# Performance work log

Measured on AMD Instinct MI355X. Metric: run time of the kernel, lower is better.

## Reference

```python
import jax, jax.numpy as jnp
import numpy as np
import math

# ---- static configuration (matches init_kwargs) ----
METADATA = [64, 48, 32]   # channels per l = 0,1,2
MAX_L = 3                 # order_out
N_BATCH = 32768
fact = math.factorial

def _cg_complex(l1, m1, l2, m2, l3, m3):
    # Clebsch-Gordan coefficient <l1 m1 l2 m2 | l3 m3> via Racah formula
    if m1 + m2 != m3 or l3 < abs(l1 - l2) or l3 > l1 + l2:
        return 0.0
    pre = math.sqrt((2*l3+1) * fact(l1+l2-l3) * fact(l1-l2+l3) * fact(-l1+l2+l3) / fact(l1+l2+l3+1))
    pre *= math.sqrt(fact(l1+m1)*fact(l1-m1)*fact(l2+m2)*fact(l2-m2)*fact(l3+m3)*fact(l3-m3))
    kmin = max(0, l2-l3-m1, l1-l3+m2)
    kmax = min(l1+l2-l3, l1-m1, l2+m2)
    s = 0.0
    for k in range(kmin, kmax+1):
        s += (-1)**k / (fact(k)*fact(l1+l2-l3-k)*fact(l1-m1-k)*fact(l2+m2-k)*fact(l3-l2+m1+k)*fact(l3-l1-m2+k))
    return pre * s

def _U(l):
    # complex->real spherical harmonic change of basis, rows = real m', cols = complex m
    U = np.zeros((2*l+1, 2*l+1), dtype=np.complex128)
    for m in range(-l, l+1):
        r = m + l
        if m > 0:
            U[r, m+l] = (-1)**m / math.sqrt(2.0); U[r, -m+l] = 1.0/math.sqrt(2.0)
        elif m == 0:
            U[r, l] = 1.0
        else:
            U[r, m+l] = 1j/math.sqrt(2.0); U[r, -m+l] = -1j*(-1)**m/math.sqrt(2.0)
    return U

def _real_cg(l1, l2, l3):
    Cc = np.zeros((2*l1+1, 2*l2+1, 2*l3+1))
    for m1 in range(-l1, l1+1):
        for m2 in range(-l2, l2+1):
            for m3 in range(-l3, l3+1):
                Cc[m1+l1, m2+l2, m3+l3] = _cg_complex(l1, m1, l2, m2, l3, m3)
    T = np.einsum('am,bn,co,mno->abc', _U(l1), _U(l2), _U(l3).conj(), Cc.astype(np.complex128))
    T = T.imag if np.abs(T.imag).max() > np.abs(T.real).max() else T.real
    return np.ascontiguousarray(T).astype(np.float32)

# ---- static index structures ----
L_IN = len(METADATA)
OFF_IN = np.concatenate([[0], np.cumsum([METADATA[l]*(2*l+1) for l in range(L_IN)])]).astype(np.int64)
DIM_IN = int(OFF_IN[-1])  # 368
PATHS = []
for l1 in range(L_IN):
    for l2 in range(L_IN):
        for l3 in range(abs(l1-l2), min(l1+l2, MAX_L)+1):
            PATHS.append((l1, l2, l3, min(METADATA[l1], METADATA[l2])))
MD_OV = [0]*(MAX_L+1)
for (_, _, l3, ch) in PATHS:
    MD_OV[l3] = max(MD_OV[l3], ch)
OFF_OUT = np.concatenate([[0], np.cumsum([MD_OV[l]*(2*l+1) for l in range(MAX_L+1)])]).astype(np.int64)
DIM_OUT = int(OFF_OUT[-1])  # 672
CG = {(l1, l2, l3): jnp.asarray(_real_cg(l1, l2, l3)) for (l1, l2, l3, _) in PATHS}

_mix_id, _scat = [], []
_base = 0
for (l1, l2, l3, ch) in PATHS:
    for i in range(ch):
        for m in range(2*l3+1):
            _mix_id.append(_base + i)
            _scat.append(int(OFF_OUT[l3]) + i*(2*l3+1) + m)
    _base += ch
MIX_ID = jnp.asarray(np.array(_mix_id, dtype=np.int64))
SCATTER = jnp.asarray(np.array(_scat, dtype=np.int64))
N_MIX = _base  # 688

_chan_in = []
_cb = 0
for l in range(L_IN):
    for i in range(METADATA[l]):
        _chan_in += [_cb + i]*(2*l+1)
    _cb += METADATA[l]
CHAN_IN = jnp.asarray(np.array(_chan_in, dtype=np.int64))
N_KEEP = _cb  # 144
_kin, _kout = [], []
for l in range(L_IN):
    cp = min(METADATA[l], MD_OV[l])
    for i in range(cp):
        for m in range(2*l+1):
            _kin.append(int(OFF_IN[l]) + i*(2*l+1) + m)
            _kout.append(int(OFF_OUT[l]) + i*(2*l+1) + m)
KEEP_IN = jnp.asarray(np.array(_kin, dtype=np.int64))
KEEP_OUT = jnp.asarray(np.array(_kout, dtype=np.int64))

SQ3 = math.sqrt(3.0)

def setup_inputs() -> dict:
    key = jax.random.key(0)
    k1, k2, k3 = jax.random.split(key, 3)
    x = jax.random.normal(k1, (N_BATCH, DIM_IN), dtype=jnp.float32)
    keep_coeff = jax.random.uniform(k2, (N_KEEP,), minval=-SQ3, maxval=SQ3, dtype=jnp.float32)
    mix_coeff = jax.random.uniform(k3, (N_MIX,), minval=-SQ3, maxval=SQ3, dtype=jnp.float32)
    return {"x": x, "keep_coeff": keep_coeff, "mix_coeff": mix_coeff}

def reference(x, keep_coeff, mix_coeff):
    n = x.shape[0]
    # keep path: per-channel coeff broadcast over m components
    x_keep = x * keep_coeff[CHAN_IN]  # [N, 368]
    # CG tensor-product self-coupling (diagonal channel pairing per path)
    tps = []
    for (l1, l2, l3, ch) in PATHS:
        x1 = x[:, OFF_IN[l1]:OFF_IN[l1]+ch*(2*l1+1)].reshape(n, ch, 2*l1+1)
        x2 = x[:, OFF_IN[l2]:OFF_IN[l2]+ch*(2*l2+1)].reshape(n, ch, 2*l2+1)
        tps.append(jnp.einsum('nia,nib,abm->nim', x1, x2, CG[(l1, l2, l3)]).reshape(n, -1))
    cat = jnp.concatenate(tps, axis=1)  # [N, 2576] non-overlapped TP output
    cat = cat * 0.5 * mix_coeff[MIX_ID]
    # scatter (index_add) into overlapped output layout
    out = jnp.zeros((n, DIM_OUT), dtype=x.dtype).at[:, SCATTER].add(cat)
    # gather + add of keep path (index_select + add_)
    out = out.at[:, KEEP_OUT].add(x_keep[:, KEEP_IN])
    return out
```

## Files before the change

kernel.cpp:

```cpp
#include <hip/hip_runtime.h>


namespace cgc {

struct cplx { double re, im; };
constexpr cplx cmul(cplx a, cplx b){ return {a.re*b.re - a.im*b.im, a.re*b.im + a.im*b.re}; }

constexpr double cfact(int n){ double r = 1.0; for (int i = 2; i <= n; ++i) r *= i; return r; }
constexpr double cabsd(double x){ return x < 0 ? -x : x; }

constexpr double csqrtd(double x){
  if (x <= 0.0) return 0.0;
  double g = x > 1.0 ? x : 1.0;
  for (int i = 0; i < 48; ++i) g = 0.5*(g + x/g);
  return g;
}

constexpr double SQRT2 = csqrtd(2.0);

constexpr double cg_complex(int l1,int m1,int l2,int m2,int l3,int m3){
  if (m1 + m2 != m3) return 0.0;
  int lo = l1 > l2 ? l1 - l2 : l2 - l1;
  if (l3 < lo || l3 > l1 + l2) return 0.0;
  double pre = csqrtd((2*l3+1) * cfact(l1+l2-l3)*cfact(l1-l2+l3)*cfact(-l1+l2+l3)/cfact(l1+l2+l3+1));
  pre *= csqrtd(cfact(l1+m1)*cfact(l1-m1)*cfact(l2+m2)*cfact(l2-m2)*cfact(l3+m3)*cfact(l3-m3));
  int kmin = 0;
  if (l2-l3-m1 > kmin) kmin = l2-l3-m1;
  if (l1-l3+m2 > kmin) kmin = l1-l3+m2;
  int kmax = l1+l2-l3;
  if (l1-m1 < kmax) kmax = l1-m1;
  if (l2+m2 < kmax) kmax = l2+m2;
  double s = 0.0;
  for (int k = kmin; k <= kmax; ++k){
    double d = cfact(k)*cfact(l1+l2-l3-k)*cfact(l1-m1-k)*cfact(l2+m2-k)
             * cfact(l3-l2+m1+k)*cfact(l3-l1-m2+k);
    s += ((k & 1) ? -1.0 : 1.0) / d;
  }
  return pre * s;
}

constexpr cplx Uent(int l, int r, int c){
  int m = r - l;
  if (m > 0){
    if (c ==  m + l) return { ((m & 1) ? -1.0 : 1.0)/SQRT2, 0.0 };
    if (c == -m + l) return { 1.0/SQRT2, 0.0 };
    return {0.0, 0.0};
  } else if (m == 0){
    if (c == l) return {1.0, 0.0};
    return {0.0, 0.0};
  } else {
    int ma = -m;
    if (c ==  m + l) return { 0.0, 1.0/SQRT2 };
    if (c == -m + l) return { 0.0, -(((ma & 1) ? -1.0 : 1.0))/SQRT2 };
    return {0.0, 0.0};
  }
}

template<int L1,int L2,int L3>
struct CGData { float w[(2*L1+1)*(2*L2+1)*(2*L3+1)]; };

template<int L1,int L2,int L3>
constexpr CGData<L1,L2,L3> make_cg(){
  constexpr int D1 = 2*L1+1, D2 = 2*L2+1, D3 = 2*L3+1;
  cplx U1[D1*D1] = {}; cplx U2[D2*D2] = {}; cplx U3c[D3*D3] = {};
  for (int r = 0; r < D1; ++r) for (int c = 0; c < D1; ++c) U1[r*D1+c] = Uent(L1, r, c);
  for (int r = 0; r < D2; ++r) for (int c = 0; c < D2; ++c) U2[r*D2+c] = Uent(L2, r, c);
  for (int r = 0; r < D3; ++r) for (int c = 0; c < D3; ++c){
    cplx u = Uent(L3, r, c); u.im = -u.im; U3c[r*D3+c] = u;
  }
  double Cc[D1*D2*D3] = {};
  for (int m1 = -L1; m1 <= L1; ++m1)
    for (int m2 = -L2; m2 <= L2; ++m2){
      int m3 = m1 + m2;
      if (m3 < -L3 || m3 > L3) continue;
      Cc[((m1+L1)*D2 + (m2+L2))*D3 + (m3+L3)] = cg_complex(L1,m1,L2,m2,L3,m3);
    }
  double re[D1*D2*D3] = {}; double im[D1*D2*D3] = {};
  for (int a = 0; a < D1; ++a)
    for (int b = 0; b < D2; ++b)
      for (int c = 0; c < D3; ++c){
        double sre = 0.0, sim = 0.0;
        for (int m = 0; m < D1; ++m)
          for (int n = 0; n < D2; ++n){
            int o = m + n - L1 - L2 + L3;
            if (o < 0 || o >= D3) continue;
            double cc = Cc[(m*D2+n)*D3 + o];
            if (cc == 0.0) continue;
            cplx p = cmul(cmul(U1[a*D1+m], U2[b*D2+n]), U3c[c*D3+o]);
            sre += p.re * cc; sim += p.im * cc;
          }
        re[(a*D2+b)*D3+c] = sre; im[(a*D2+b)*D3+c] = sim;
      }
  double mre = 0.0, mim = 0.0;
  for (int k = 0; k < D1*D2*D3; ++k){
    if (cabsd(re[k]) > mre) mre = cabsd(re[k]);
    if (cabsd(im[k]) > mim) mim = cabsd(im[k]);
  }
  CGData<L1,L2,L3> outv{};
  for (int k = 0; k < D1*D2*D3; ++k){
    double v = (mim > mre) ? im[k] : re[k];
    outv.w[k] = (cabsd(v) < 1e-10) ? 0.0f : (float)v;
  }
  return outv;
}

}

template<int L1,int L2,int L3>
__device__ __forceinline__ void tp_path(const float* xa, const float* xb, float cmix, float* acc){
  constexpr cgc::CGData<L1,L2,L3> cg = cgc::make_cg<L1,L2,L3>();
  constexpr int D1 = 2*L1+1, D2 = 2*L2+1, D3 = 2*L3+1;
  #pragma unroll
  for (int a = 0; a < D1; ++a){
    #pragma unroll
    for (int b = 0; b < D2; ++b){
      const float pr = xa[a] * xb[b];
      #pragma unroll
      for (int m = 0; m < D3; ++m){
        const float W = cg.w[(a*D2+b)*D3 + m];
        if (W != 0.0f) acc[m] += (cmix * W) * pr;
      }
    }
  }
}


constexpr int RPB      = 4;
constexpr int IN_DIM   = 368;
constexpr int OUT_DIM  = 672;
constexpr int OUT_PAD  = 676;

__global__ __launch_bounds__(256, 4) void selfmix_kernel(
    const float* __restrict__ x, const float* __restrict__ keep,
    const float* __restrict__ mix, float* __restrict__ out, int n)
{
  __shared__ float sin_[RPB * IN_DIM];
  __shared__ float sout[RPB * OUT_PAD];

  const int tid  = threadIdx.x;
  const int rb   = blockIdx.x * RPB;
  const int rows = (n - rb < RPB) ? (n - rb) : RPB;

  {
    const float4* gx = (const float4*)(x + (size_t)rb * IN_DIM);
    float4* s4 = (float4*)sin_;
    const int nf4 = rows * (IN_DIM / 4);
    for (int t = tid; t < nf4; t += 256) s4[t] = gx[t];
  }
  __syncthreads();

  if (tid < 128){
    const int row = tid >> 5;
    const int i   = tid & 31;
    if (row < rows){
      const float* xr = sin_ + row * IN_DIM;
      float*     orow = sout + row * OUT_PAD;
      const float s = xr[i];
      float p[3], d[5];
      #pragma unroll
      for (int k = 0; k < 3; ++k) p[k] = xr[64 + i*3 + k];
      #pragma unroll
      for (int k = 0; k < 5; ++k) d[k] = xr[208 + i*5 + k];

      float o0 = 0.f;
      float o1[3] = {0.f,0.f,0.f};
      float o2[5] = {0.f,0.f,0.f,0.f,0.f};
      float o3[7] = {0.f,0.f,0.f,0.f,0.f,0.f,0.f};

      tp_path<0,0,0>(&s,&s, 0.5f*mix[  0+i], &o0);
      tp_path<0,1,1>(&s, p, 0.5f*mix[ 64+i],  o1);
      tp_path<0,2,2>(&s, d, 0.5f*mix[112+i],  o2);
      tp_path<1,0,1>( p,&s, 0.5f*mix[144+i],  o1);
      tp_path<1,1,0>( p, p, 0.5f*mix[192+i], &o0);
      tp_path<1,1,1>( p, p, 0.5f*mix[240+i],  o1);
      tp_path<1,1,2>( p, p, 0.5f*mix[288+i],  o2);
      tp_path<1,2,1>( p, d, 0.5f*mix[336+i],  o1);
      tp_path<1,2,2>( p, d, 0.5f*mix[368+i],  o2);
      tp_path<1,2,3>( p, d, 0.5f*mix[400+i],  o3);
      tp_path<2,0,2>( d,&s, 0.5f*mix[432+i],  o2);
      tp_path<2,1,1>( d, p, 0.5f*mix[464+i],  o1);
      tp_path<2,1,2>( d, p, 0.5f*mix[496+i],  o2);
      tp_path<2,1,3>( d, p, 0.5f*mix[528+i],  o3);
      tp_path<2,2,0>( d, d, 0.5f*mix[560+i], &o0);
      tp_path<2,2,1>( d, d, 0.5f*mix[592+i],  o1);
      tp_path<2,2,2>( d, d, 0.5f*mix[624+i],  o2);
      tp_path<2,2,3>( d, d, 0.5f*mix[656+i],  o3);

      o0 += keep[i] * s;
      const float k1 = keep[64+i], k2 = keep[112+i];
      #pragma unroll
      for (int k = 0; k < 3; ++k) o1[k] += k1 * p[k];
      #pragma unroll
      for (int k = 0; k < 5; ++k) o2[k] += k2 * d[k];

      orow[i] = o0;
      #pragma unroll
      for (int k = 0; k < 3; ++k) orow[ 64 + i*3 + k] = o1[k];
      #pragma unroll
      for (int k = 0; k < 5; ++k) orow[208 + i*5 + k] = o2[k];
      #pragma unroll
      for (int k = 0; k < 7; ++k) orow[448 + i*7 + k] = o3[k];
    }
  } else if (tid < 192){
    const int u   = tid - 128;
    const int row = u >> 4;
    const int i   = 32 + (u & 15);
    if (row < rows){
      const float* xr = sin_ + row * IN_DIM;
      float*     orow = sout + row * OUT_PAD;
      const float s = xr[i];
      float p[3];
      #pragma unroll
      for (int k = 0; k < 3; ++k) p[k] = xr[64 + i*3 + k];

      float o0 = 0.f;
      float o1[3] = {0.f,0.f,0.f};
      float o2[5] = {0.f,0.f,0.f,0.f,0.f};

      tp_path<0,0,0>(&s,&s, 0.5f*mix[  0+i], &o0);
      tp_path<0,1,1>(&s, p, 0.5f*mix[ 64+i],  o1);
      tp_path<1,0,1>( p,&s, 0.5f*mix[144+i],  o1);
      tp_path<1,1,0>( p, p, 0.5f*mix[192+i], &o0);
      tp_path<1,1,1>( p, p, 0.5f*mix[240+i],  o1);
      tp_path<1,1,2>( p, p, 0.5f*mix[288+i],  o2);

      o0 += keep[i] * s;
      const float k1 = keep[64+i];
      #pragma unroll
      for (int k = 0; k < 3; ++k) o1[k] += k1 * p[k];

      orow[i] = o0;
      #pragma unroll
      for (int k = 0; k < 3; ++k) orow[ 64 + i*3 + k] = o1[k];
      #pragma unroll
      for (int k = 0; k < 5; ++k) orow[208 + i*5 + k] = o2[k];
    }
  } else {
    const int u   = tid - 192;
    const int row = u >> 4;
    const int i   = 48 + (u & 15);
    if (row < rows){
      const float s = sin_[row * IN_DIM + i];
      float o0 = 0.f;
      tp_path<0,0,0>(&s,&s, 0.5f*mix[0+i], &o0);
      o0 += keep[i] * s;
      sout[row * OUT_PAD + i] = o0;
    }
  }
  __syncthreads();

  {
    float4* gout = (float4*)(out + (size_t)rb * OUT_DIM);
    const float4* so4 = (const float4*)sout;
    const int nf4 = rows * (OUT_DIM / 4);
    for (int t = tid; t < nf4; t += 256){
      const int r = t / 168;
      const int j = t - r * 168;
      gout[t] = so4[r * 169 + j];
    }
  }
}

extern "C" void kernel_launch(void* const* d_in, const int* in_sizes, int n_in,
                              void* d_out, int out_size, void* d_ws, size_t ws_size,
                              hipStream_t stream)
{
  const float* x    = (const float*)d_in[0];
  const float* keep = (const float*)d_in[1];
  const float* mix  = (const float*)d_in[2];
  float* out = (float*)d_out;
  const int n = in_sizes[0] / IN_DIM;
  const int blocks = (n + RPB - 1) / RPB;
  selfmix_kernel<<<blocks, 256, 0, stream>>>(x, keep, mix, out, n);
}
```

Before: 149.4 us.

## Read inputs directly from global memory, drop input LDS staging and barrier

Removes the shared-memory staging buffer for input rows and its barrier, so each thread loads its x components directly from global memory. It also hoists the mix and keep coefficient loads ahead of the path computations and raises the launch-bounds occupancy hint from 4 to 8 blocks. The aim is lower LDS use, one fewer synchronisation, and more blocks resident at once. The cost is strided, uncoalesced global loads (stride 3 and 5 floats per thread) and possibly tighter register limits.

```diff
diff --git a/kernel.cpp b/kernel.cpp
--- a/kernel.cpp
+++ b/kernel.cpp
@@ -130,30 +130,21 @@
 constexpr int OUT_DIM  = 672;
 constexpr int OUT_PAD  = 676;
 
-__global__ __launch_bounds__(256, 4) void selfmix_kernel(
+__global__ __launch_bounds__(256, 8) void selfmix_kernel(
     const float* __restrict__ x, const float* __restrict__ keep,
     const float* __restrict__ mix, float* __restrict__ out, int n)
 {
-  __shared__ float sin_[RPB * IN_DIM];
   __shared__ float sout[RPB * OUT_PAD];
 
   const int tid  = threadIdx.x;
   const int rb   = blockIdx.x * RPB;
   const int rows = (n - rb < RPB) ? (n - rb) : RPB;
-
-  {
-    const float4* gx = (const float4*)(x + (size_t)rb * IN_DIM);
-    float4* s4 = (float4*)sin_;
-    const int nf4 = rows * (IN_DIM / 4);
-    for (int t = tid; t < nf4; t += 256) s4[t] = gx[t];
-  }
-  __syncthreads();
 
   if (tid < 128){
     const int row = tid >> 5;
     const int i   = tid & 31;
     if (row < rows){
-      const float* xr = sin_ + row * IN_DIM;
+      const float* xr = x + (size_t)(rb + row) * IN_DIM;
       float*     orow = sout + row * OUT_PAD;
       const float s = xr[i];
       float p[3], d[5];
@@ -161,33 +152,39 @@
       for (int k = 0; k < 3; ++k) p[k] = xr[64 + i*3 + k];
       #pragma unroll
       for (int k = 0; k < 5; ++k) d[k] = xr[208 + i*5 + k];
+      const float c000 = 0.5f*mix[  0+i], c011 = 0.5f*mix[ 64+i], c022 = 0.5f*mix[112+i];
+      const float c101 = 0.5f*mix[144+i], c110 = 0.5f*mix[192+i], c111 = 0.5f*mix[240+i];
+      const float c112 = 0.5f*mix[288+i], c121 = 0.5f*mix[336+i], c122 = 0.5f*mix[368+i];
+      const float c123 = 0.5f*mix[400+i], c202 = 0.5f*mix[432+i], c211 = 0.5f*mix[464+i];
+      const float c212 = 0.5f*mix[496+i], c213 = 0.5f*mix[528+i], c220 = 0.5f*mix[560+i];
+      const float c221 = 0.5f*mix[592+i], c222 = 0.5f*mix[624+i], c223 = 0.5f*mix[656+i];
+      const float k0 = keep[i], k1 = keep[64+i], k2 = keep[112+i];
 
       float o0 = 0.f;
       float o1[3] = {0.f,0.f,0.f};
       float o2[5] = {0.f,0.f,0.f,0.f,0.f};
       float o3[7] = {0.f,0.f,0.f,0.f,0.f,0.f,0.f};
 
-      tp_path<0,0,0>(&s,&s, 0.5f*mix[  0+i], &o0);
-      tp_path<0,1,1>(&s, p, 0.5f*mix[ 64+i],  o1);
-      tp_path<0,2,2>(&s, d, 0.5f*mix[112+i],  o2);
-      tp_path<1,0,1>( p,&s, 0.5f*mix[144+i],  o1);
-      tp_path<1,1,0>( p, p, 0.5f*mix[192+i], &o0);
-      tp_path<1,1,1>( p, p, 0.5f*mix[240+i],  o1);
-      tp_path<1,1,2>( p, p, 0.5f*mix[288+i],  o2);
-      tp_path<1,2,1>( p, d, 0.5f*mix[336+i],  o1);
-      tp_path<1,2,2>( p, d, 0.5f*mix[368+i],  o2);
-      tp_path<1,2,3>( p, d, 0.5f*mix[400+i],  o3);
-      tp_path<2,0,2>( d,&s, 0.5f*mix[432+i],  o2);
-      tp_path<2,1,1>( d, p, 0.5f*mix[464+i],  o1);
-      tp_path<2,1,2>( d, p, 0.5f*mix[496+i],  o2);
-      tp_path<2,1,3>( d, p, 0.5f*mix[528+i],  o3);
-      tp_path<2,2,0>( d, d, 0.5f*mix[560+i], &o0);
-      tp_path<2,2,1>( d, d, 0.5f*mix[592+i],  o1);
-      tp_path<2,2,2>( d, d, 0.5f*mix[624+i],  o2);
-      tp_path<2,2,3>( d, d, 0.5f*mix[656+i],  o3);
-
-      o0 += keep[i] * s;
-      const float k1 = keep[64+i], k2 = keep[112+i];
+      tp_path<0,0,0>(&s,&s, c000, &o0);
+      tp_path<0,1,1>(&s, p, c011,  o1);
+      tp_path<0,2,2>(&s, d, c022,  o2);
+      tp_path<1,0,1>( p,&s, c101,  o1);
+      tp_path<1,1,0>( p, p, c110, &o0);
+      tp_path<1,1,1>( p, p, c111,  o1);
+      tp_path<1,1,2>( p, p, c112,  o2);
+      tp_path<1,2,1>( p, d, c121,  o1);
+      tp_path<1,2,2>( p, d, c122,  o2);
+      tp_path<1,2,3>( p, d, c123,  o3);
+      tp_path<2,0,2>( d,&s, c202,  o2);
+      tp_path<2,1,1>( d, p, c211,  o1);
+      tp_path<2,1,2>( d, p, c212,  o2);
+      tp_path<2,1,3>( d, p, c213,  o3);
+      tp_path<2,2,0>( d, d, c220, &o0);
+      tp_path<2,2,1>( d, d, c221,  o1);
+      tp_path<2,2,2>( d, d, c222,  o2);
+      tp_path<2,2,3>( d, d, c223,  o3);
+
+      o0 += k0 * s;
       #pragma unroll
       for (int k = 0; k < 3; ++k) o1[k] += k1 * p[k];
       #pragma unroll
@@ -206,7 +203,7 @@
     const int row = u >> 4;
     const int i   = 32 + (u & 15);
     if (row < rows){
-      const float* xr = sin_ + row * IN_DIM;
+      const float* xr = x + (size_t)(rb + row) * IN_DIM;
       float*     orow = sout + row * OUT_PAD;
       const float s = xr[i];
       float p[3];
@@ -240,7 +237,7 @@
     const int row = u >> 4;
     const int i   = 48 + (u & 15);
     if (row < rows){
-      const float s = sin_[row * IN_DIM + i];
+      const float s = x[(size_t)(rb + row) * IN_DIM + i];
       float o0 = 0.f;
       tp_path<0,0,0>(&s,&s, 0.5f*mix[0+i], &o0);
       o0 += keep[i] * s;
```

After: 289.4 us. 1.94x slower.
